# Performance work log

Measured on AMD Instinct MI355X. Metric: run time of the kernel, lower is better.

Reference implementation:

```python
import jax, jax.numpy as jnp
import numpy as np

QLEN, MLEN, BSZ, D_MODEL, N_HEAD, D_HEAD = 512, 512, 16, 1024, 16, 64
KLEN = QLEN + MLEN
EPS = 1e-5


def setup_inputs() -> dict:
    key = jax.random.key(0)
    ks = jax.random.split(key, 9)
    s = 0.02
    w = jax.random.normal(ks[0], (QLEN, BSZ, D_MODEL), jnp.float32)
    r = jax.random.normal(ks[1], (KLEN, D_MODEL), jnp.float32)
    r_w_bias = jax.random.normal(ks[2], (N_HEAD, D_HEAD), jnp.float32) * s
    r_r_bias = jax.random.normal(ks[3], (N_HEAD, D_HEAD), jnp.float32) * s
    mems = jax.random.normal(ks[4], (MLEN, BSZ, D_MODEL), jnp.float32)
    # causal mask with memory: position i can attend to keys j <= i + MLEN
    i = np.arange(QLEN)[:, None]
    j = np.arange(KLEN)[None, :]
    attn_mask = jnp.asarray(j > i + MLEN)  # True = masked, [qlen, klen]
    Wqkv = jax.random.normal(ks[5], (D_MODEL, 3 * N_HEAD * D_HEAD), jnp.float32) * s
    Wr = jax.random.normal(ks[6], (D_MODEL, N_HEAD * D_HEAD), jnp.float32) * s
    Wo = jax.random.normal(ks[7], (N_HEAD * D_HEAD, D_MODEL), jnp.float32) * s
    gamma = jnp.ones((D_MODEL,), jnp.float32)
    beta = jnp.zeros((D_MODEL,), jnp.float32)
    return {"w": w, "r": r, "r_w_bias": r_w_bias, "r_r_bias": r_r_bias,
            "mems": mems, "attn_mask": attn_mask, "Wqkv": Wqkv, "Wr": Wr,
            "Wo": Wo, "gamma": gamma, "beta": beta}


def _rel_shift(x):
    # x: [qlen, klen, bsz, n_head] -> Transformer-XL relative shift
    q, k, b, n = x.shape
    x = jnp.pad(x, ((0, 0), (1, 0), (0, 0), (0, 0)))  # [q, k+1, b, n]
    x = x.reshape(k + 1, q, b, n)[1:]                  # drop first row
    return x.reshape(q, k, b, n)


def _layer_norm(x, gamma, beta):
    mu = jnp.mean(x, axis=-1, keepdims=True)
    var = jnp.mean(jnp.square(x - mu), axis=-1, keepdims=True)
    return (x - mu) * jax.lax.rsqrt(var + EPS) * gamma + beta


def reference(w, r, r_w_bias, r_r_bias, mems, attn_mask, Wqkv, Wr, Wo, gamma, beta):
    qlen, bsz = w.shape[0], w.shape[1]
    scale = 1.0 / (D_HEAD ** 0.5)

    cat = jnp.concatenate([mems, w], axis=0)          # [klen, b, d]
    w_heads = cat @ Wqkv                               # [klen, b, 3*n*d]
    r_head_k = (r @ Wr).reshape(-1, N_HEAD, D_HEAD)    # [rlen, n, d]
    q, k, v = jnp.split(w_heads, 3, axis=-1)
    klen = k.shape[0]
    q = q[-qlen:].reshape(qlen, bsz, N_HEAD, D_HEAD)
    k = k.reshape(klen, bsz, N_HEAD, D_HEAD)
    v = v.reshape(klen, bsz, N_HEAD, D_HEAD)

    AC = jnp.einsum('ibnd,jbnd->ijbn', q + r_w_bias, k)
    BD = jnp.einsum('ibnd,jnd->ijbn', q + r_r_bias, r_head_k)
    BD = _rel_shift(BD)
    attn_score = (AC + BD) * scale                     # [q, k, b, n]
    attn_score = jnp.where(attn_mask[:, :, None, None], -jnp.inf, attn_score)
    attn_prob = jax.nn.softmax(attn_score, axis=1)

    attn_vec = jnp.einsum('ijbn,jbnd->ibnd', attn_prob, v)
    attn_vec = attn_vec.reshape(qlen, bsz, N_HEAD * D_HEAD)
    attn_out = attn_vec @ Wo                           # [q, b, d_model]
    return _layer_norm(w + attn_out, gamma, beta)      # post-lnorm path
```

## Files before the change

kernel.cpp:

```cpp
#include <hip/hip_runtime.h>
#include <hip/hip_bf16.h>

#define QLENC 512
#define MLENC 512
#define KLENC 1024
#define BSZC 16
#define NHEADC 16

typedef __attribute__((ext_vector_type(8))) short bf16x8;
typedef __attribute__((ext_vector_type(4))) float f32x4;

__device__ __forceinline__ float bf2f(short u) {
    union { unsigned u; float f; } c;
    c.u = ((unsigned)(unsigned short)u) << 16;
    return c.f;
}
__device__ __forceinline__ short f2bf(float x) {
    union { float f; unsigned u; } c; c.f = x;
    unsigned r = (c.u + 0x7fffu + ((c.u >> 16) & 1u)) >> 16;
    return (short)r;
}
__device__ __forceinline__ int cvtpk(float a, float b) {
    int r;
    asm("v_cvt_pk_bf16_f32 %0, %1, %2" : "=v"(r) : "v"(a), "v"(b));
    return r;
}
__device__ __forceinline__ int pack2(short a, short b) {
    return (int)((unsigned)(unsigned short)a | (((unsigned)(unsigned short)b) << 16));
}
__device__ __forceinline__ void gload_lds16(const void* g, void* l) {
    auto* gp = reinterpret_cast<const __attribute__((address_space(1))) unsigned int*>(
        reinterpret_cast<unsigned long long>(g));
    auto* lp = reinterpret_cast<__attribute__((address_space(3))) unsigned int*>(
        reinterpret_cast<unsigned long long>(l));
    __builtin_amdgcn_global_load_lds(gp, lp, 16, 0, 0);
}

__launch_bounds__(256)
__global__ void cvt_k(const float* __restrict__ in0, const float* __restrict__ in1,
                      short* __restrict__ out, int n0, int ntot)
{
    int idx = (blockIdx.x * 256 + threadIdx.x) * 8;
    if (idx >= ntot) return;
    const float* src = (idx < n0) ? (in0 + idx) : (in1 + (idx - n0));
    f32x4 a = *(const f32x4*)src;
    f32x4 b = *(const f32x4*)(src + 4);
    int4 v;
    v.x = cvtpk(a[0], a[1]); v.y = cvtpk(a[2], a[3]);
    v.z = cvtpk(b[0], b[1]); v.w = cvtpk(b[2], b[3]);
    *(int4*)(out + idx) = v;
}

__launch_bounds__(256)
__global__ void tr_k(const float* __restrict__ in, short* __restrict__ out,
                     int K, int N)
{
    __shared__ float T[64][65];
    const int k0 = blockIdx.x * 64, n0 = blockIdx.y * 64;
    const int t = threadIdx.x;
    const int rr = t >> 4, cc = (t & 15) * 4;
#pragma unroll
    for (int it = 0; it < 4; ++it) {
        int r = it * 16 + rr;
        f32x4 v = *(const f32x4*)(in + (size_t)(k0 + r) * N + n0 + cc);
        T[r][cc] = v[0]; T[r][cc + 1] = v[1]; T[r][cc + 2] = v[2]; T[r][cc + 3] = v[3];
    }
    __syncthreads();
    const int orow = t >> 2, kseg = (t & 3) * 16;
    int y[8];
#pragma unroll
    for (int j = 0; j < 8; ++j)
        y[j] = cvtpk(T[kseg + 2 * j][orow], T[kseg + 2 * j + 1][orow]);
    short* dst = out + (size_t)(n0 + orow) * K + k0 + kseg;
    *(int4*)dst       = *(int4*)&y[0];
    *(int4*)(dst + 8) = *(int4*)&y[4];
}

template<int MODE>
__launch_bounds__(256)
__global__ void gemm_k(const short* __restrict__ A, const short* __restrict__ BT,
                       const short* __restrict__ A2, const short* __restrict__ BT2,
                       short* __restrict__ o4,
                       short* __restrict__ o0,
                       short* __restrict__ o2, short* __restrict__ o3,
                       int K)
{
    __shared__ short As[2][128 * 32];
    __shared__ short Bs[2][128 * 32];

    const int tid  = threadIdx.x;
    const int lane = tid & 63, wid = tid >> 6;
    const int g = lane >> 4, li = lane & 15;
    const int wr = wid >> 1, wc = wid & 1;

    int m_tile, n_tile;
    bool isR = false;
    const short* Ap = A;
    const short* Bp = BT;
    if (MODE == 0) {
        if (blockIdx.x >= 2560) {
            isR = true;
            int i2 = blockIdx.x - 2560;
            m_tile = i2 >> 3; n_tile = i2 & 7;
            Ap = A2; Bp = BT2;
        } else {
            int xcd = blockIdx.x & 7;
            int idx = blockIdx.x >> 3;
            if (idx < 64) {
                m_tile = 64 + xcd * 8 + (idx & 7);
                n_tile = idx >> 3;
            } else {
                int i2 = idx - 64;
                int half = i2 >> 7, rem = i2 & 127;
                m_tile = xcd * 16 + half * 8 + (rem & 7);
                n_tile = 8 + (rem >> 3);
            }
        }
    } else {
        int xcd = blockIdx.x & 7;
        int idx = blockIdx.x >> 3;
        m_tile = xcd * 8 + (idx & 7);
        n_tile = idx >> 3;
    }
    const int m_base = m_tile * 128, n_base = n_tile * 128;

    f32x4 acc[4][4];
    const f32x4 z4 = {0.f, 0.f, 0.f, 0.f};
#pragma unroll
    for (int a = 0; a < 4; ++a)
#pragma unroll
        for (int c = 0; c < 4; ++c) acc[a][c] = z4;

    const int lrow = lane >> 2;
    const int lchk = (lane & 3) ^ (lrow & 3) ^ ((lane >> 4) & 3);
    const int rc = (g ^ (li & 3) ^ ((li >> 2) & 3)) * 8;

    const short* Ab = Ap + (size_t)(m_base + 32 * wid + lrow) * K + lchk * 8;
    const short* Bb = Bp + (size_t)(n_base + 32 * wid + lrow) * K + lchk * 8;
    const int lbase = 32 * wid;

#pragma unroll
    for (int h = 0; h < 2; ++h) {
        gload_lds16(Ab + (size_t)(16 * h) * K, &As[0][(lbase + 16 * h) * 32]);
        gload_lds16(Bb + (size_t)(16 * h) * K, &Bs[0][(lbase + 16 * h) * 32]);
    }
    asm volatile("s_waitcnt vmcnt(0)" ::: "memory");
    __syncthreads();

    const int nsteps = K >> 5;
    int cur = 0;
    for (int t = 0; t < nsteps; ++t) {
        if (t + 1 < nsteps) {
            const int k0n = (t + 1) * 32;
#pragma unroll
            for (int h = 0; h < 2; ++h) {
                gload_lds16(Ab + (size_t)(16 * h) * K + k0n, &As[cur ^ 1][(lbase + 16 * h) * 32]);
                gload_lds16(Bb + (size_t)(16 * h) * K + k0n, &Bs[cur ^ 1][(lbase + 16 * h) * 32]);
            }
        }
        bf16x8 af[4], bfv[4];
#pragma unroll
        for (int mf = 0; mf < 4; ++mf)
            af[mf] = *(const bf16x8*)&As[cur][(wr * 64 + mf * 16 + li) * 32 + rc];
#pragma unroll
        for (int nf = 0; nf < 4; ++nf)
            bfv[nf] = *(const bf16x8*)&Bs[cur][(wc * 64 + nf * 16 + li) * 32 + rc];
        __builtin_amdgcn_s_setprio(1);
#pragma unroll
        for (int mf = 0; mf < 4; ++mf)
#pragma unroll
            for (int nf = 0; nf < 4; ++nf)
                acc[mf][nf] = __builtin_amdgcn_mfma_f32_16x16x32_bf16(af[mf], bfv[nf], acc[mf][nf], 0, 0, 0);
        __builtin_amdgcn_s_setprio(0);
        __syncthreads();
        cur ^= 1;
    }

#pragma unroll
    for (int mf = 0; mf < 4; ++mf) {
#pragma unroll
        for (int nf = 0; nf < 4; ++nf) {
#pragma unroll
            for (int q = 0; q < 4; ++q) {
                int m   = m_base + wr * 64 + mf * 16 + 4 * g + q;
                int col = n_base + wc * 64 + nf * 16 + li;
                float v = acc[mf][nf][q];
                if (MODE == 0) {
                    if (isR) {
                        int h = col >> 6, d = col & 63;
                        o4[((h * KLENC + m) << 6) + d] = f2bf(v);
                    } else {
                        int t = m >> 4, b = m & 15;
                        int sec = col >> 10, h = (col >> 6) & 15, d = col & 63;
                        if (sec == 0) {
                            if (t >= MLENC) {
                                int i = t - MLENC;
                                int off = (((b * NHEADC + h) * QLENC + i) << 6) + d;
                                o0[off] = f2bf(v);
                            }
                        } else {
                            int off = (((b * NHEADC + h) * KLENC + t) << 6) + d;
                            if (sec == 1) o2[off] = f2bf(v); else o3[off] = f2bf(v);
                        }
                    }
                } else {
                    o0[(size_t)m * 1024 + col] = f2bf(v);
                }
            }
        }
    }
}

__launch_bounds__(256)
__global__ void attn_k(const short* __restrict__ qs,
                       const float* __restrict__ rwb, const float* __restrict__ rrb,
                       const short* __restrict__ kk, const short* __restrict__ vv,
                       const short* __restrict__ rkm, short* __restrict__ ctx)
{
    __shared__ short Kb[2][32 * 64];
    __shared__ short Rl[128 * 64];
    __shared__ short Vt[2][64 * 40];
    __shared__ short Pl[4][16 * 44];

    const int tid  = threadIdx.x;
    const int lane = tid & 63, wid = tid >> 6;
    const int g = lane >> 4, li = lane & 15;

    const int bid = blockIdx.x;
    const int xcd = bid & 7;
    const int idx = bid >> 3;
    const int pid = xcd * 32 + (idx >> 3);
    const int blk = idx & 7;
    const int n = pid >> 4, b = pid & 15;

    const int i0 = blk * 64, i0w = i0 + wid * 16;
    const int bn = b * NHEADC + n;
    const int jjlo0 = 448 - i0;

    const int l8 = lane >> 3;
    const int l7 = lane & 7;
    const int lc = l7 ^ l8;
    const int dt = tid & 63, jh = wid * 8;

    const short* qsp = qs + (size_t)(bn * QLENC + i0w + li) * 64;
    bf16x8 q0 = *(const bf16x8*)(qsp + g * 8);
    bf16x8 q1 = *(const bf16x8*)(qsp + 32 + g * 8);
    const float* bwp = rwb + n * 64;
    const float* brp = rrb + n * 64;
    bf16x8 qwf[2], qrf[2];
#pragma unroll
    for (int e = 0; e < 8; ++e) {
        float v0 = bf2f(q0[e]), v1 = bf2f(q1[e]);
        qwf[0][e] = f2bf(v0 + bwp[g * 8 + e]);
        qwf[1][e] = f2bf(v1 + bwp[32 + g * 8 + e]);
        qrf[0][e] = f2bf(v0 + brp[g * 8 + e]);
        qrf[1][e] = f2bf(v1 + brp[32 + g * 8 + e]);
    }

    const f32x4 z4 = {0.f, 0.f, 0.f, 0.f};
    f32x4 o[4];
    float srun[4];
#pragma unroll
    for (int nf = 0; nf < 4; ++nf) o[nf] = z4;
#pragma unroll
    for (int q = 0; q < 4; ++q) srun[q] = 0.f;

    const int nch = (i0 + 607) >> 5;
    const int pswz = (g ^ (li & 7)) * 8;
    const int rbase = 48 - wid * 16;
    const float SCL = 0.125f * 1.44269504f;

    gload_lds16(kk + ((size_t)bn * 1024 + 8 * wid + l8) * 64 + lc * 8,
                &Kb[0][wid * 512]);
#pragma unroll
    for (int q = 0; q < 3; ++q) {
        int lr = 32 * q + 8 * wid + l8;
        int srow = jjlo0 + lr; if (srow > 1023) srow = 1023;
        gload_lds16(rkm + ((size_t)n * 1024 + srow) * 64 + lc * 8,
                    &Rl[((32 * q + 8 * wid) & 127) * 64]);
    }
    short va0, va1, va2, va3, va4, va5, va6, va7;
    {
        const short* vb = vv + ((size_t)bn * 1024 + jh) * 64 + dt;
        va0 = vb[0];      va1 = vb[64];     va2 = vb[2 * 64]; va3 = vb[3 * 64];
        va4 = vb[4 * 64]; va5 = vb[5 * 64]; va6 = vb[6 * 64]; va7 = vb[7 * 64];
    }
    int cur = 0;

    for (int ch = 0; ch < nch; ++ch) {
        const int j0 = ch * 32;
        {
            int4 vw; vw.x = pack2(va0, va1); vw.y = pack2(va2, va3);
            vw.z = pack2(va4, va5); vw.w = pack2(va6, va7);
            *(int4*)&Vt[cur][dt * 40 + jh] = vw;
        }
        asm volatile("s_waitcnt vmcnt(0)" ::: "memory");
        __syncthreads();
        if (ch + 1 < nch) {
            const int j0n = j0 + 32;
            gload_lds16(kk + ((size_t)bn * 1024 + j0n + 8 * wid + l8) * 64 + lc * 8,
                        &Kb[cur ^ 1][wid * 512]);
            int lr = 96 + 32 * ch + 8 * wid + l8;
            int srow = jjlo0 + lr; if (srow > 1023) srow = 1023;
            gload_lds16(rkm + ((size_t)n * 1024 + srow) * 64 + lc * 8,
                        &Rl[((96 + 32 * ch + 8 * wid) & 127) * 64]);
            const short* vb = vv + ((size_t)bn * 1024 + j0n + jh) * 64 + dt;
            va0 = vb[0];      va1 = vb[64];     va2 = vb[2 * 64]; va3 = vb[3 * 64];
            va4 = vb[4 * 64]; va5 = vb[5 * 64]; va6 = vb[6 * 64]; va7 = vb[7 * 64];
        }

        const short* kbuf = &Kb[cur][0];
        f32x4 sc[2];
        __builtin_amdgcn_s_setprio(1);
#pragma unroll
        for (int nf = 0; nf < 2; ++nf) {
            bf16x8 k0f = *(const bf16x8*)&kbuf[(nf * 16 + li) * 64 + pswz];
            bf16x8 k1f = *(const bf16x8*)&kbuf[(nf * 16 + li) * 64 + (pswz ^ 32)];
            f32x4 t = __builtin_amdgcn_mfma_f32_16x16x32_bf16(qwf[0], k0f, z4, 0, 0, 0);
            sc[nf] = __builtin_amdgcn_mfma_f32_16x16x32_bf16(qwf[1], k1f, t, 0, 0, 0);
        }
        const int rsh = 32 * ch;
        f32x4 bd[3];
#pragma unroll
        for (int nf = 0; nf < 3; ++nf) {
            int prow = (rbase + nf * 16 + li + rsh) & 127;
            bf16x8 r0f = *(const bf16x8*)&Rl[prow * 64 + pswz];
            bf16x8 r1f = *(const bf16x8*)&Rl[prow * 64 + (pswz ^ 32)];
            f32x4 t = __builtin_amdgcn_mfma_f32_16x16x32_bf16(qrf[0], r0f, z4, 0, 0, 0);
            bd[nf] = __builtin_amdgcn_mfma_f32_16x16x32_bf16(qrf[1], r1f, t, 0, 0, 0);
        }
        __builtin_amdgcn_s_setprio(0);

        float p0v[4], p1v[4];
#pragma unroll
        for (int q = 0; q < 4; ++q) {
            int r  = 4 * g + q;
            int i  = i0w + r;
            int cc = 15 + li - r;
            int src = (lane & 48) | (cc & 15);
            float b0 = __shfl(bd[0][q], src);
            float b1 = __shfl(bd[1][q], src);
            float b2 = __shfl(bd[2][q], src);
            float bd0 = (cc < 16) ? b0 : b1;
            float bd1 = (cc < 16) ? b1 : b2;
            float s0 = (sc[0][q] + bd0) * SCL;
            float s1 = (sc[1][q] + bd1) * SCL;
            if (j0 + li > i + MLENC)      s0 = -1e30f;
            if (j0 + 16 + li > i + MLENC) s1 = -1e30f;
            float p0 = exp2f(s0);
            float p1 = exp2f(s1);
            srun[q] += p0 + p1;
            p0v[q] = p0; p1v[q] = p1;
        }

        short* pw = &Pl[wid][0];
#pragma unroll
        for (int q = 0; q < 4; ++q) {
            int pr = cvtpk(p0v[q], p1v[q]);
            pw[(4 * g + q) * 44 + li]      = (short)(pr & 0xffff);
            pw[(4 * g + q) * 44 + 16 + li] = (short)(((unsigned)pr) >> 16);
        }
        bf16x8 pa = *(const bf16x8*)&pw[li * 44 + g * 8];
        __builtin_amdgcn_s_setprio(1);
#pragma unroll
        for (int nf = 0; nf < 4; ++nf) {
            bf16x8 vf = *(const bf16x8*)&Vt[cur][(nf * 16 + li) * 40 + g * 8];
            o[nf] = __builtin_amdgcn_mfma_f32_16x16x32_bf16(pa, vf, o[nf], 0, 0, 0);
        }
        __builtin_amdgcn_s_setprio(0);
        cur ^= 1;
    }

    float inv[4];
#pragma unroll
    for (int q = 0; q < 4; ++q) {
        float s = srun[q];
#pragma unroll
        for (int off = 1; off < 16; off <<= 1) s += __shfl_xor(s, off);
        inv[q] = 1.0f / s;
    }
#pragma unroll
    for (int nf = 0; nf < 4; ++nf)
#pragma unroll
        for (int q = 0; q < 4; ++q) {
            int i = i0w + 4 * g + q;
            ctx[(size_t)(i * BSZC + b) * 1024 + n * 64 + nf * 16 + li] = f2bf(o[nf][q] * inv[q]);
        }
}

__launch_bounds__(256)
__global__ void ln_k(const short* __restrict__ attn, const float* __restrict__ win,
                     const float* __restrict__ gamma, const float* __restrict__ beta,
                     float* __restrict__ out)
{
    const int wid = threadIdx.x >> 6, lane = threadIdx.x & 63;
    const int m = blockIdx.x * 4 + wid;
    const short* ap = attn + (size_t)m * 1024 + lane * 16;
    const float* wp = win + (size_t)m * 1024 + lane * 16;

    bf16x8 A0 = *(const bf16x8*)(ap);
    bf16x8 A1 = *(const bf16x8*)(ap + 8);
    f32x4 W[4];
#pragma unroll
    for (int t = 0; t < 4; ++t) W[t] = *(const f32x4*)(wp + 4 * t);

    float x[16];
#pragma unroll
    for (int e = 0; e < 8; ++e) {
        x[e]     = bf2f(A0[e]) + W[e >> 2][e & 3];
        x[e + 8] = bf2f(A1[e]) + W[2 + (e >> 2)][e & 3];
    }

    float s = 0.f;
#pragma unroll
    for (int e = 0; e < 16; ++e) s += x[e];
#pragma unroll
    for (int off = 1; off < 64; off <<= 1) s += __shfl_xor(s, off);
    float mu = s * (1.0f / 1024.0f);
    float vs = 0.f;
#pragma unroll
    for (int e = 0; e < 16; ++e) { float dd = x[e] - mu; vs += dd * dd; }
#pragma unroll
    for (int off = 1; off < 64; off <<= 1) vs += __shfl_xor(vs, off);
    float rstd = rsqrtf(vs * (1.0f / 1024.0f) + 1e-5f);

    f32x4 G[4], Bt[4];
#pragma unroll
    for (int t = 0; t < 4; ++t) {
        G[t]  = *(const f32x4*)(gamma + lane * 16 + 4 * t);
        Bt[t] = *(const f32x4*)(beta + lane * 16 + 4 * t);
    }
#pragma unroll
    for (int t = 0; t < 4; ++t) {
        f32x4 y;
#pragma unroll
        for (int c = 0; c < 4; ++c)
            y[c] = (x[4 * t + c] - mu) * rstd * G[t][c] + Bt[t][c];
        *(f32x4*)(out + (size_t)m * 1024 + lane * 16 + 4 * t) = y;
    }
}

extern "C" void kernel_launch(void* const* d_in, const int* in_sizes, int n_in,
                              void* d_out, int out_size, void* d_ws, size_t ws_size,
                              hipStream_t stream)
{
    const float* w     = (const float*)d_in[0];
    const float* r     = (const float*)d_in[1];
    const float* rwb   = (const float*)d_in[2];
    const float* rrb   = (const float*)d_in[3];
    const float* mems  = (const float*)d_in[4];
    const float* Wqkv  = (const float*)d_in[6];
    const float* Wr    = (const float*)d_in[7];
    const float* Wo    = (const float*)d_in[8];
    const float* gamma = (const float*)d_in[9];
    const float* beta  = (const float*)d_in[10];
    float* out = (float*)d_out;

    char* p = (char*)d_ws;
    short* qws   = (short*)p; p += (size_t)BSZC * NHEADC * QLENC * 64 * 2;
    short* kks   = (short*)p; p += (size_t)BSZC * NHEADC * KLENC * 64 * 2;
    short* vvs   = (short*)p; p += (size_t)BSZC * NHEADC * KLENC * 64 * 2;
    short* rks   = (short*)p; p += (size_t)NHEADC * KLENC * 64 * 2;
    short* WqkvT = (short*)p; p += (size_t)3072 * 1024 * 2;
    short* rbf   = (short*)p; p += (size_t)1024 * 1024 * 2;
    short* WrT   = (short*)p; p += (size_t)1024 * 1024 * 2;
    short* WoT   = (short*)p; p += (size_t)1024 * 1024 * 2;
    short* Abf = (short*)d_out;
    short* ctx = (short*)d_out;
    short* att = (short*)d_ws;

    cvt_k<<<8192, 256, 0, stream>>>(mems, w, Abf, 8388608, 16777216);
    cvt_k<<<512, 256, 0, stream>>>(r, r, rbf, 1048576, 1048576);
    tr_k<<<dim3(16, 48), 256, 0, stream>>>(Wqkv, WqkvT, 1024, 3072);
    tr_k<<<dim3(16, 16), 256, 0, stream>>>(Wr, WrT, 1024, 1024);
    tr_k<<<dim3(16, 16), 256, 0, stream>>>(Wo, WoT, 1024, 1024);

    gemm_k<0><<<2624, 256, 0, stream>>>(Abf, WqkvT, rbf, WrT, rks,
                                        qws, kks, vvs, 1024);
    attn_k<<<2048, 256, 0, stream>>>(qws, rwb, rrb, kks, vvs, rks, ctx);
    gemm_k<2><<<512, 256, 0, stream>>>(ctx, WoT, nullptr, nullptr, nullptr,
                                       att, nullptr, nullptr, 1024);
    ln_k<<<2048, 256, 0, stream>>>(att, w, gamma, beta, out);
}
```

Baseline: 340.9 us.

## Double attention query tile to 128 rows with 8 warps and split loaders

```diff
diff --git a/kernel.cpp b/kernel.cpp
--- a/kernel.cpp
+++ b/kernel.cpp
@@ -211,16 +211,16 @@
     }
 }
 
-__launch_bounds__(256)
+__launch_bounds__(512)
 __global__ void attn_k(const short* __restrict__ qs,
                        const float* __restrict__ rwb, const float* __restrict__ rrb,
                        const short* __restrict__ kk, const short* __restrict__ vv,
                        const short* __restrict__ rkm, short* __restrict__ ctx)
 {
     __shared__ short Kb[2][32 * 64];
-    __shared__ short Rl[128 * 64];
+    __shared__ short Rl[192 * 64];
     __shared__ short Vt[2][64 * 40];
-    __shared__ short Pl[4][16 * 44];
+    __shared__ short Pl[8][16 * 40];
 
     const int tid  = threadIdx.x;
     const int lane = tid & 63, wid = tid >> 6;
@@ -229,18 +229,18 @@
     const int bid = blockIdx.x;
     const int xcd = bid & 7;
     const int idx = bid >> 3;
-    const int pid = xcd * 32 + (idx >> 3);
-    const int blk = idx & 7;
+    const int pid = xcd * 32 + (idx >> 2);
+    const int blk = idx & 3;
     const int n = pid >> 4, b = pid & 15;
 
-    const int i0 = blk * 64, i0w = i0 + wid * 16;
+    const int i0 = blk * 128, i0w = i0 + wid * 16;
     const int bn = b * NHEADC + n;
-    const int jjlo0 = 448 - i0;
+    const int jjlo0 = 384 - i0;
 
     const int l8 = lane >> 3;
     const int l7 = lane & 7;
     const int lc = l7 ^ l8;
-    const int dt = tid & 63, jh = wid * 8;
+    const int dt = tid & 63, jh = (tid >> 6) * 8;
 
     const short* qsp = qs + (size_t)(bn * QLENC + i0w + li) * 64;
     bf16x8 q0 = *(const bf16x8*)(qsp + g * 8);
@@ -265,31 +265,34 @@
 #pragma unroll
     for (int q = 0; q < 4; ++q) srun[q] = 0.f;
 
-    const int nch = (i0 + 607) >> 5;
+    const int nch = 4 * blk + 20;
     const int pswz = (g ^ (li & 7)) * 8;
-    const int rbase = 48 - wid * 16;
+    const int rbase = 112 - 16 * wid;
     const float SCL = 0.125f * 1.44269504f;
 
-    gload_lds16(kk + ((size_t)bn * 1024 + 8 * wid + l8) * 64 + lc * 8,
-                &Kb[0][wid * 512]);
-#pragma unroll
-    for (int q = 0; q < 3; ++q) {
-        int lr = 32 * q + 8 * wid + l8;
-        int srow = jjlo0 + lr; if (srow > 1023) srow = 1023;
-        gload_lds16(rkm + ((size_t)n * 1024 + srow) * 64 + lc * 8,
-                    &Rl[((32 * q + 8 * wid) & 127) * 64]);
-    }
     short va0, va1, va2, va3, va4, va5, va6, va7;
-    {
+    if (wid < 4) {
+        gload_lds16(kk + ((size_t)bn * 1024 + 8 * wid + l8) * 64 + lc * 8,
+                    &Kb[0][wid * 512]);
         const short* vb = vv + ((size_t)bn * 1024 + jh) * 64 + dt;
         va0 = vb[0];      va1 = vb[64];     va2 = vb[2 * 64]; va3 = vb[3 * 64];
         va4 = vb[4 * 64]; va5 = vb[5 * 64]; va6 = vb[6 * 64]; va7 = vb[7 * 64];
+    } else {
+        const int w4 = wid - 4;
+#pragma unroll
+        for (int q = 0; q < 5; ++q) {
+            int lr = 32 * q + 8 * w4;
+            int srow = jjlo0 + lr + l8; if (srow > 1023) srow = 1023;
+            gload_lds16(rkm + ((size_t)n * 1024 + srow) * 64 + lc * 8,
+                        &Rl[lr * 64]);
+        }
     }
     int cur = 0;
+    int bs = 0;
 
     for (int ch = 0; ch < nch; ++ch) {
         const int j0 = ch * 32;
-        {
+        if (wid < 4) {
             int4 vw; vw.x = pack2(va0, va1); vw.y = pack2(va2, va3);
             vw.z = pack2(va4, va5); vw.w = pack2(va6, va7);
             *(int4*)&Vt[cur][dt * 40 + jh] = vw;
@@ -297,16 +300,21 @@
         asm volatile("s_waitcnt vmcnt(0)" ::: "memory");
         __syncthreads();
         if (ch + 1 < nch) {
-            const int j0n = j0 + 32;
-            gload_lds16(kk + ((size_t)bn * 1024 + j0n + 8 * wid + l8) * 64 + lc * 8,
-                        &Kb[cur ^ 1][wid * 512]);
-            int lr = 96 + 32 * ch + 8 * wid + l8;
-            int srow = jjlo0 + lr; if (srow > 1023) srow = 1023;
-            gload_lds16(rkm + ((size_t)n * 1024 + srow) * 64 + lc * 8,
-                        &Rl[((96 + 32 * ch + 8 * wid) & 127) * 64]);
-            const short* vb = vv + ((size_t)bn * 1024 + j0n + jh) * 64 + dt;
-            va0 = vb[0];      va1 = vb[64];     va2 = vb[2 * 64]; va3 = vb[3 * 64];
-            va4 = vb[4 * 64]; va5 = vb[5 * 64]; va6 = vb[6 * 64]; va7 = vb[7 * 64];
+            if (wid < 4) {
+                const int j0n = j0 + 32;
+                gload_lds16(kk + ((size_t)bn * 1024 + j0n + 8 * wid + l8) * 64 + lc * 8,
+                            &Kb[cur ^ 1][wid * 512]);
+                const short* vb = vv + ((size_t)bn * 1024 + j0n + jh) * 64 + dt;
+                va0 = vb[0];      va1 = vb[64];     va2 = vb[2 * 64]; va3 = vb[3 * 64];
+                va4 = vb[4 * 64]; va5 = vb[5 * 64]; va6 = vb[6 * 64]; va7 = vb[7 * 64];
+            } else {
+                const int w4 = wid - 4;
+                int sp0 = bs + 160; if (sp0 >= 192) sp0 -= 192;
+                int srow = jjlo0 + 160 + 32 * ch + 8 * w4 + l8;
+                if (srow > 1023) srow = 1023;
+                gload_lds16(rkm + ((size_t)n * 1024 + srow) * 64 + lc * 8,
+                            &Rl[(sp0 + 8 * w4) * 64]);
+            }
         }
 
         const short* kbuf = &Kb[cur][0];
@@ -319,11 +327,11 @@
             f32x4 t = __builtin_amdgcn_mfma_f32_16x16x32_bf16(qwf[0], k0f, z4, 0, 0, 0);
             sc[nf] = __builtin_amdgcn_mfma_f32_16x16x32_bf16(qwf[1], k1f, t, 0, 0, 0);
         }
-        const int rsh = 32 * ch;
         f32x4 bd[3];
 #pragma unroll
         for (int nf = 0; nf < 3; ++nf) {
-            int prow = (rbase + nf * 16 + li + rsh) & 127;
+            int prow = bs + rbase + nf * 16 + li;
+            if (prow >= 192) prow -= 192;
             bf16x8 r0f = *(const bf16x8*)&Rl[prow * 64 + pswz];
             bf16x8 r1f = *(const bf16x8*)&Rl[prow * 64 + (pswz ^ 32)];
             f32x4 t = __builtin_amdgcn_mfma_f32_16x16x32_bf16(qrf[0], r0f, z4, 0, 0, 0);
@@ -331,11 +339,11 @@
         }
         __builtin_amdgcn_s_setprio(0);
 
+        const bool needMask = (j0 + 31 > i0w + MLENC);
         float p0v[4], p1v[4];
 #pragma unroll
         for (int q = 0; q < 4; ++q) {
             int r  = 4 * g + q;
-            int i  = i0w + r;
             int cc = 15 + li - r;
             int src = (lane & 48) | (cc & 15);
             float b0 = __shfl(bd[0][q], src);
@@ -345,8 +353,11 @@
             float bd1 = (cc < 16) ? b1 : b2;
             float s0 = (sc[0][q] + bd0) * SCL;
             float s1 = (sc[1][q] + bd1) * SCL;
-            if (j0 + li > i + MLENC)      s0 = -1e30f;
-            if (j0 + 16 + li > i + MLENC) s1 = -1e30f;
+            if (needMask) {
+                int i = i0w + r;
+                if (j0 + li > i + MLENC)      s0 = -1e30f;
+                if (j0 + 16 + li > i + MLENC) s1 = -1e30f;
+            }
             float p0 = exp2f(s0);
             float p1 = exp2f(s1);
             srun[q] += p0 + p1;
@@ -357,10 +368,10 @@
 #pragma unroll
         for (int q = 0; q < 4; ++q) {
             int pr = cvtpk(p0v[q], p1v[q]);
-            pw[(4 * g + q) * 44 + li]      = (short)(pr & 0xffff);
-            pw[(4 * g + q) * 44 + 16 + li] = (short)(((unsigned)pr) >> 16);
-        }
-        bf16x8 pa = *(const bf16x8*)&pw[li * 44 + g * 8];
+            pw[(4 * g + q) * 40 + li]      = (short)(pr & 0xffff);
+            pw[(4 * g + q) * 40 + 16 + li] = (short)(((unsigned)pr) >> 16);
+        }
+        bf16x8 pa = *(const bf16x8*)&pw[li * 40 + g * 8];
         __builtin_amdgcn_s_setprio(1);
 #pragma unroll
         for (int nf = 0; nf < 4; ++nf) {
@@ -369,6 +380,7 @@
         }
         __builtin_amdgcn_s_setprio(0);
         cur ^= 1;
+        bs += 32; if (bs >= 192) bs -= 192;
     }
 
     float inv[4];
@@ -477,7 +489,7 @@
 
     gemm_k<0><<<2624, 256, 0, stream>>>(Abf, WqkvT, rbf, WrT, rks,
                                         qws, kks, vvs, 1024);
-    attn_k<<<2048, 256, 0, stream>>>(qws, rwb, rrb, kks, vvs, rks, ctx);
+    attn_k<<<1024, 512, 0, stream>>>(qws, rwb, rrb, kks, vvs, rks, ctx);
     gemm_k<2><<<512, 256, 0, stream>>>(ctx, WoT, nullptr, nullptr, nullptr,
                                        att, nullptr, nullptr, 1024);
     ln_k<<<2048, 256, 0, stream>>>(att, w, gamma, beta, out);
```

Result: faster. 305.4 us (-10.4%).
